# Kernel optimization log

Measured on AMD Instinct MI355X. Metric: run time of the kernel, lower is better.

Reference implementation:

```python
import jax, jax.numpy as jnp
import numpy as np

N_NODES = 10000
N_EDGES = 640000
N_GRAPHS = 64
IN_FEATS = 128
H_FEATS = 128


def setup_inputs() -> dict:
    key = jax.random.key(0)
    ks = jax.random.split(key, 8)
    in_feat = jax.random.normal(ks[0], (N_NODES, IN_FEATS), dtype=jnp.float32)
    src = jax.random.randint(ks[1], (N_EDGES,), 0, N_NODES, dtype=jnp.int32)
    dst = jax.random.randint(ks[2], (N_EDGES,), 0, N_NODES, dtype=jnp.int32)
    graph_ids = jnp.sort(jax.random.randint(ks[3], (N_NODES,), 0, N_GRAPHS, dtype=jnp.int32))
    s1 = 1.0 / np.sqrt(IN_FEATS)
    s2 = 1.0 / np.sqrt(H_FEATS)
    W1 = jax.random.uniform(ks[4], (IN_FEATS, H_FEATS), jnp.float32, -s1, s1)
    b1 = jnp.zeros((H_FEATS,), jnp.float32)
    W2 = jax.random.uniform(ks[5], (H_FEATS, H_FEATS), jnp.float32, -s2, s2)
    b2 = jnp.zeros((H_FEATS,), jnp.float32)
    Wd = jax.random.uniform(ks[6], (H_FEATS, 1), jnp.float32, -s2, s2)
    bd = jnp.zeros((1,), jnp.float32)
    return {"in_feat": in_feat, "src": src, "dst": dst, "graph_ids": graph_ids,
            "W1": W1, "b1": b1, "W2": W2, "b2": b2, "Wd": Wd, "bd": bd}


def _graph_conv(x, src, dst, norm_src, norm_dst, W, b):
    # DGL GraphConv, norm='both': D_dst^{-1/2} A D_src^{-1/2} X W + b
    x = x * norm_src[:, None]
    agg = jax.ops.segment_sum(x[src], dst, num_segments=N_NODES)  # scatter-add over edges
    agg = agg * norm_dst[:, None]
    return agg @ W + b


def reference(in_feat, src, dst, graph_ids, W1, b1, W2, b2, Wd, bd):
    ones_e = jnp.ones((N_EDGES,), in_feat.dtype)
    out_deg = jax.ops.segment_sum(ones_e, src, num_segments=N_NODES)
    in_deg = jax.ops.segment_sum(ones_e, dst, num_segments=N_NODES)
    norm_src = jnp.where(out_deg > 0, out_deg, 1.0) ** -0.5
    norm_dst = jnp.where(in_deg > 0, in_deg, 1.0) ** -0.5

    h = jax.nn.relu(_graph_conv(in_feat, src, dst, norm_src, norm_dst, W1, b1))
    h = jax.nn.relu(_graph_conv(h, src, dst, norm_src, norm_dst, W2, b2))

    # dgl.mean_nodes: per-graph mean of node features
    counts = jax.ops.segment_sum(jnp.ones((N_NODES,), h.dtype), graph_ids, num_segments=N_GRAPHS)
    pooled = jax.ops.segment_sum(h, graph_ids, num_segments=N_GRAPHS)
    pooled = pooled / jnp.maximum(counts, 1.0)[:, None]

    out = pooled @ Wd + bd  # [G, 1]
    return out.squeeze(-1)
```

## Files before the change

kernel.cpp:

```cpp
#include <hip/hip_runtime.h>
#include <hip/hip_fp16.h>

#define N_NODES 10000
#define N_EDGES 640000
#define N_GRAPHS 64
#define FEATS 128

#define NSLICE 64
#define EPS (N_EDGES / NSLICE)
#define CAP 128
#define PRE_BLOCKS 1250

static inline size_t align_up(size_t x, size_t a) { return (x + a - 1) & ~(a - 1); }

__global__ __launch_bounds__(256) void hist_kernel(const int* __restrict__ src,
                                                   const int* __restrict__ dst,
                                                   unsigned short* __restrict__ counts,
                                                   unsigned short* __restrict__ scounts,
                                                   int* __restrict__ graph_cnt,
                                                   float* __restrict__ graph_sum) {
    __shared__ int h[N_NODES];
    const int tid = threadIdx.x;
    const int b = blockIdx.x;
    if (b == 0 && tid < 2 * N_GRAPHS) {
        if (tid < N_GRAPHS) graph_cnt[tid] = 0;
        else                graph_sum[tid - N_GRAPHS] = 0.f;
    }
    const bool is_dst = (b < NSLICE);
    const int slice = is_dst ? b : b - NSLICE;
    const int* col = is_dst ? dst : src;
    unsigned short* outp = (is_dst ? counts : scounts) + slice * N_NODES;

    for (int i = tid; i < N_NODES; i += 256) h[i] = 0;
    __syncthreads();
    const int4* c4 = (const int4*)(col + slice * EPS);
    for (int i = tid; i < EPS / 4; i += 256) {
        int4 v = c4[i];
        atomicAdd(&h[v.x], 1);
        atomicAdd(&h[v.y], 1);
        atomicAdd(&h[v.z], 1);
        atomicAdd(&h[v.w], 1);
    }
    __syncthreads();
    for (int i = tid; i < N_NODES; i += 256) outp[i] = (unsigned short)h[i];
}

__global__ __launch_bounds__(256) void degnorm_base_kernel(const unsigned short* __restrict__ counts,
                                                           const unsigned short* __restrict__ scounts,
                                                           const int* __restrict__ gids,
                                                           int* __restrict__ bases,
                                                           int* __restrict__ deg_in,
                                                           float* __restrict__ norm_src,
                                                           float* __restrict__ norm_dst,
                                                           int* __restrict__ graph_cnt) {
    __shared__ int gcnt[N_GRAPHS];
    const int tid = threadIdx.x;
    if (tid < N_GRAPHS) gcnt[tid] = 0;
    __syncthreads();
    int n = blockIdx.x * 256 + tid;
    if (n < N_NODES) {
        int run = n * CAP;
        for (int s = 0; s < NSLICE; s++) {
            int c = counts[s * N_NODES + n];
            bases[s * N_NODES + n] = run;
            run += c;
        }
        int di = run - n * CAP;
        int dou = 0;
        for (int s = 0; s < NSLICE; s++) dou += scounts[s * N_NODES + n];
        deg_in[n] = di;
        norm_dst[n] = rsqrtf((float)(di < 1 ? 1 : di));
        norm_src[n] = rsqrtf((float)(dou < 1 ? 1 : dou));
        atomicAdd(&gcnt[gids[n]], 1);
    }
    __syncthreads();
    if (tid < N_GRAPHS && gcnt[tid]) atomicAdd(&graph_cnt[tid], gcnt[tid]);
}

__global__ __launch_bounds__(256) void scatter_prescale_kernel(const int* __restrict__ src,
                                                               const int* __restrict__ dst,
                                                               const int* __restrict__ bases,
                                                               int* __restrict__ sorted_src,
                                                               const float* __restrict__ in_feat,
                                                               const float* __restrict__ norm_src,
                                                               __half* __restrict__ xs) {
    const int tid = threadIdx.x;
    if (blockIdx.x < NSLICE) {
        __shared__ int cur[N_NODES];
        const int s = blockIdx.x;
        for (int i = tid; i < N_NODES; i += 256) cur[i] = bases[s * N_NODES + i];
        __syncthreads();
        const int4* s4 = (const int4*)(src + s * EPS);
        const int4* d4 = (const int4*)(dst + s * EPS);
        for (int i = tid; i < EPS / 4; i += 256) {
            int4 sv = s4[i];
            int4 dv = d4[i];
            int p;
            p = atomicAdd(&cur[dv.x], 1); sorted_src[p] = sv.x;
            p = atomicAdd(&cur[dv.y], 1); sorted_src[p] = sv.y;
            p = atomicAdd(&cur[dv.z], 1); sorted_src[p] = sv.z;
            p = atomicAdd(&cur[dv.w], 1); sorted_src[p] = sv.w;
        }
    } else {
        int i = (blockIdx.x - NSLICE) * 256 + tid;
        if (i < N_NODES * (FEATS / 4)) {
            int n = i >> 5;
            float4 v = ((const float4*)in_feat)[i];
            float s = norm_src[n];
            __half2 h0 = __floats2half2_rn(v.x * s, v.y * s);
            __half2 h1 = __floats2half2_rn(v.z * s, v.w * s);
            __half2* o = (__half2*)(xs + (size_t)i * 4);
            o[0] = h0; o[1] = h1;
        }
    }
}

__global__ __launch_bounds__(256) void aggregate_kernel(const __half* __restrict__ X,
                                                        const int* __restrict__ sorted_src,
                                                        const int* __restrict__ deg_in,
                                                        const float* __restrict__ norm_dst,
                                                        __half* __restrict__ out) {
    const int tid = threadIdx.x;
    const int wave = tid >> 6, lane = tid & 63;
    const int grp = lane >> 4, l16 = lane & 15;
    const int n = blockIdx.x * 4 + wave;
    const int start = n * CAP;
    const int cnt = deg_in[n];
    const uint4* __restrict__ x4 = (const uint4*)X;
    float acc[8] = {0.f, 0.f, 0.f, 0.f, 0.f, 0.f, 0.f, 0.f};

    int c = grp;
    for (; c + 12 < cnt; c += 16) {
        int idx[4];
#pragma unroll
        for (int k = 0; k < 4; k++) idx[k] = sorted_src[start + c + 4 * k];
        uint4 v[4];
#pragma unroll
        for (int k = 0; k < 4; k++) v[k] = x4[idx[k] * 16 + l16];
#pragma unroll
        for (int k = 0; k < 4; k++) {
            const __half2* hp = (const __half2*)&v[k];
#pragma unroll
            for (int j = 0; j < 4; j++) {
                float2 f = __half22float2(hp[j]);
                acc[2 * j]     += f.x;
                acc[2 * j + 1] += f.y;
            }
        }
    }
    for (; c < cnt; c += 4) {
        uint4 v = x4[sorted_src[start + c] * 16 + l16];
        const __half2* hp = (const __half2*)&v;
#pragma unroll
        for (int j = 0; j < 4; j++) {
            float2 f = __half22float2(hp[j]);
            acc[2 * j]     += f.x;
            acc[2 * j + 1] += f.y;
        }
    }
#pragma unroll
    for (int j = 0; j < 8; j++) {
        acc[j] += __shfl_xor(acc[j], 16);
        acc[j] += __shfl_xor(acc[j], 32);
    }
    if (grp == 0) {
        const float nd = norm_dst[n];
        __half2 o[4];
#pragma unroll
        for (int j = 0; j < 4; j++)
            o[j] = __floats2half2_rn(acc[2 * j] * nd, acc[2 * j + 1] * nd);
        *(uint4*)(out + (size_t)n * FEATS + l16 * 8) = *(const uint4*)o;
    }
}

__device__ __forceinline__ void stage_fp16_tile(const __half* __restrict__ A,
                                                int nb, int tid, float* As) {
    const int row = tid >> 4, c16 = tid & 15;
    uint4 v = *(const uint4*)(A + (size_t)(nb + row) * FEATS + c16 * 8);
    const __half2* hp = (const __half2*)&v;
    float* dst = As + row * FEATS + c16 * 8;
#pragma unroll
    for (int j = 0; j < 4; j++) {
        float2 f = __half22float2(hp[j]);
        dst[2 * j]     = f.x;
        dst[2 * j + 1] = f.y;
    }
}

__global__ __launch_bounds__(256) void gemm_relu_scale_kernel(const __half* __restrict__ A,
                                                              const float* __restrict__ W,
                                                              const float* __restrict__ bias,
                                                              const float* __restrict__ scale,
                                                              __half* __restrict__ out) {
    __shared__ float As[16 * FEATS];
    int tid = threadIdx.x;
    int nb = blockIdx.x * 16;
    stage_fp16_tile(A, nb, tid, As);
    __syncthreads();
    int fg = (tid & 31) << 2;
    int r  = tid >> 5;
    const float* a0p = As + r * FEATS;
    const float* a1p = As + (r + 8) * FEATS;
    float4 acc0 = make_float4(0.f, 0.f, 0.f, 0.f);
    float4 acc1 = make_float4(0.f, 0.f, 0.f, 0.f);
#pragma unroll 4
    for (int k = 0; k < FEATS; k++) {
        float a0 = a0p[k];
        float a1 = a1p[k];
        float4 w = *(const float4*)(W + k * FEATS + fg);
        acc0.x = fmaf(a0, w.x, acc0.x); acc0.y = fmaf(a0, w.y, acc0.y);
        acc0.z = fmaf(a0, w.z, acc0.z); acc0.w = fmaf(a0, w.w, acc0.w);
        acc1.x = fmaf(a1, w.x, acc1.x); acc1.y = fmaf(a1, w.y, acc1.y);
        acc1.z = fmaf(a1, w.z, acc1.z); acc1.w = fmaf(a1, w.w, acc1.w);
    }
    float4 bb = *(const float4*)(bias + fg);
    int gn0 = nb + r, gn1 = nb + r + 8;
    float s0 = scale[gn0], s1 = scale[gn1];
    __half2 h00 = __floats2half2_rn(fmaxf(acc0.x + bb.x, 0.f) * s0,
                                    fmaxf(acc0.y + bb.y, 0.f) * s0);
    __half2 h01 = __floats2half2_rn(fmaxf(acc0.z + bb.z, 0.f) * s0,
                                    fmaxf(acc0.w + bb.w, 0.f) * s0);
    __half2 h10 = __floats2half2_rn(fmaxf(acc1.x + bb.x, 0.f) * s1,
                                    fmaxf(acc1.y + bb.y, 0.f) * s1);
    __half2 h11 = __floats2half2_rn(fmaxf(acc1.z + bb.z, 0.f) * s1,
                                    fmaxf(acc1.w + bb.w, 0.f) * s1);
    __half2* o0 = (__half2*)(out + (size_t)gn0 * FEATS + fg);
    __half2* o1 = (__half2*)(out + (size_t)gn1 * FEATS + fg);
    o0[0] = h00; o0[1] = h01;
    o1[0] = h10; o1[1] = h11;
}

__global__ __launch_bounds__(256) void gemm_relu_pool_kernel(const __half* __restrict__ A,
                                                             const float* __restrict__ W,
                                                             const float* __restrict__ bias,
                                                             const float* __restrict__ Wd,
                                                             const int* __restrict__ gids,
                                                             float* __restrict__ graph_sum) {
    __shared__ float As[16 * FEATS];
    __shared__ float bins[N_GRAPHS];
    int tid = threadIdx.x;
    int nb = blockIdx.x * 16;
    stage_fp16_tile(A, nb, tid, As);
    if (tid < N_GRAPHS) bins[tid] = 0.f;
    __syncthreads();
    int fg = (tid & 31) << 2;
    int r  = tid >> 5;
    const float* a0p = As + r * FEATS;
    const float* a1p = As + (r + 8) * FEATS;
    float4 acc0 = make_float4(0.f, 0.f, 0.f, 0.f);
    float4 acc1 = make_float4(0.f, 0.f, 0.f, 0.f);
#pragma unroll 4
    for (int k = 0; k < FEATS; k++) {
        float a0 = a0p[k];
        float a1 = a1p[k];
        float4 w = *(const float4*)(W + k * FEATS + fg);
        acc0.x = fmaf(a0, w.x, acc0.x); acc0.y = fmaf(a0, w.y, acc0.y);
        acc0.z = fmaf(a0, w.z, acc0.z); acc0.w = fmaf(a0, w.w, acc0.w);
        acc1.x = fmaf(a1, w.x, acc1.x); acc1.y = fmaf(a1, w.y, acc1.y);
        acc1.z = fmaf(a1, w.z, acc1.z); acc1.w = fmaf(a1, w.w, acc1.w);
    }
    float4 bb = *(const float4*)(bias + fg);
    float4 wd = *(const float4*)(Wd + fg);
    float p0 = fmaxf(acc0.x + bb.x, 0.f) * wd.x + fmaxf(acc0.y + bb.y, 0.f) * wd.y +
               fmaxf(acc0.z + bb.z, 0.f) * wd.z + fmaxf(acc0.w + bb.w, 0.f) * wd.w;
    float p1 = fmaxf(acc1.x + bb.x, 0.f) * wd.x + fmaxf(acc1.y + bb.y, 0.f) * wd.y +
               fmaxf(acc1.z + bb.z, 0.f) * wd.z + fmaxf(acc1.w + bb.w, 0.f) * wd.w;
#pragma unroll
    for (int d = 16; d >= 1; d >>= 1) {
        p0 += __shfl_down(p0, d);
        p1 += __shfl_down(p1, d);
    }
    if ((tid & 31) == 0) {
        int gn0 = nb + r, gn1 = nb + r + 8;
        atomicAdd(&bins[gids[gn0]], p0);
        atomicAdd(&bins[gids[gn1]], p1);
    }
    __syncthreads();
    if (tid < N_GRAPHS) {
        float v = bins[tid];
        if (v != 0.f) atomicAdd(&graph_sum[tid], v);
    }
}

__global__ __launch_bounds__(64) void final_kernel(const float* __restrict__ graph_sum,
                                                   const int* __restrict__ graph_cnt,
                                                   const float* __restrict__ bd,
                                                   float* __restrict__ out) {
    int g = threadIdx.x;
    if (g < N_GRAPHS) {
        out[g] = graph_sum[g] / fmaxf((float)graph_cnt[g], 1.f) + bd[0];
    }
}

extern "C" void kernel_launch(void* const* d_in, const int* in_sizes, int n_in,
                              void* d_out, int out_size, void* d_ws, size_t ws_size,
                              hipStream_t stream) {
    const float* in_feat = (const float*)d_in[0];
    const int*   src     = (const int*)d_in[1];
    const int*   dst     = (const int*)d_in[2];
    const int*   gids    = (const int*)d_in[3];
    const float* W1      = (const float*)d_in[4];
    const float* b1      = (const float*)d_in[5];
    const float* W2      = (const float*)d_in[6];
    const float* b2      = (const float*)d_in[7];
    const float* Wd      = (const float*)d_in[8];
    const float* bd      = (const float*)d_in[9];
    float* out = (float*)d_out;

    char* ws = (char*)d_ws;
    size_t off = 0;
    int* graph_cnt = (int*)(ws + off); off += N_GRAPHS * 4;
    float* graph_sum = (float*)(ws + off); off += N_GRAPHS * 4;
    off = align_up(off, 512);
    unsigned short* counts  = (unsigned short*)(ws + off); off += (size_t)NSLICE * N_NODES * 2;
    off = align_up(off, 512);
    unsigned short* scounts = (unsigned short*)(ws + off); off += (size_t)NSLICE * N_NODES * 2;
    off = align_up(off, 512);
    int* bases = (int*)(ws + off); off += (size_t)NSLICE * N_NODES * 4;
    off = align_up(off, 512);
    int* deg_in  = (int*)(ws + off); off += N_NODES * 4;
    off = align_up(off, 512);
    float* norm_src = (float*)(ws + off); off += N_NODES * 4;
    off = align_up(off, 512);
    float* norm_dst = (float*)(ws + off); off += N_NODES * 4;
    off = align_up(off, 512);
    int* sorted_src = (int*)(ws + off); off += (size_t)N_NODES * CAP * 4 + 4096;
    off = align_up(off, 512);
    __half* xs   = (__half*)(ws + off); off += (size_t)N_NODES * FEATS * 2;
    off = align_up(off, 512);
    __half* h    = (__half*)(ws + off); off += (size_t)N_NODES * FEATS * 2;
    off = align_up(off, 512);
    __half* agg1 = (__half*)(ws + off); off += (size_t)N_NODES * FEATS * 2;
    off = align_up(off, 512);
    __half* agg2 = (__half*)(ws + off); off += (size_t)N_NODES * FEATS * 2;
    (void)ws_size;

    hist_kernel<<<2 * NSLICE, 256, 0, stream>>>(src, dst, counts, scounts,
                                                graph_cnt, graph_sum);
    degnorm_base_kernel<<<(N_NODES + 255) / 256, 256, 0, stream>>>(counts, scounts, gids,
                                                                   bases, deg_in, norm_src,
                                                                   norm_dst, graph_cnt);
    scatter_prescale_kernel<<<NSLICE + PRE_BLOCKS, 256, 0, stream>>>(src, dst, bases,
                                                                     sorted_src, in_feat,
                                                                     norm_src, xs);

    aggregate_kernel<<<N_NODES / 4, 256, 0, stream>>>(xs, sorted_src, deg_in, norm_dst, agg1);
    gemm_relu_scale_kernel<<<N_NODES / 16, 256, 0, stream>>>(agg1, W1, b1, norm_src, h);

    aggregate_kernel<<<N_NODES / 4, 256, 0, stream>>>(h, sorted_src, deg_in, norm_dst, agg2);
    gemm_relu_pool_kernel<<<N_NODES / 16, 256, 0, stream>>>(agg2, W2, b2, Wd, gids, graph_sum);

    final_kernel<<<1, 64, 0, stream>>>(graph_sum, graph_cnt, bd, out);
}
```

Measured before the change: 168.8 us.

## Fuse neighbor aggregation into the GEMM kernels and double histogram slices

Each layer's gather-aggregate is merged into the GEMM kernel. Every wave aggregates 4 destination nodes straight into the fp32 shared tile, so the fp16 agg1/agg2 intermediate buffers and two kernel launches go away. NSLICE is doubled to 128, which spreads the histogram and scatter work across more blocks, and degnorm is relaunched with 64-thread blocks to get more blocks. The trade-offs: the fused kernels launch only 625 blocks, each wave handles 4 nodes in sequence, so gather parallelism drops. The extra slices also make degnorm's serial per-node loop twice as long.

Result: no change. 169.3 us (+0.3%).

```diff
diff --git a/kernel.cpp b/kernel.cpp
--- a/kernel.cpp
+++ b/kernel.cpp
@@ -6,7 +6,7 @@
 #define N_GRAPHS 64
 #define FEATS 128
 
-#define NSLICE 64
+#define NSLICE 128
 #define EPS (N_EDGES / NSLICE)
 #define CAP 128
 #define PRE_BLOCKS 1250
@@ -45,19 +45,19 @@
     for (int i = tid; i < N_NODES; i += 256) outp[i] = (unsigned short)h[i];
 }
 
-__global__ __launch_bounds__(256) void degnorm_base_kernel(const unsigned short* __restrict__ counts,
-                                                           const unsigned short* __restrict__ scounts,
-                                                           const int* __restrict__ gids,
-                                                           int* __restrict__ bases,
-                                                           int* __restrict__ deg_in,
-                                                           float* __restrict__ norm_src,
-                                                           float* __restrict__ norm_dst,
-                                                           int* __restrict__ graph_cnt) {
+__global__ __launch_bounds__(64) void degnorm_base_kernel(const unsigned short* __restrict__ counts,
+                                                          const unsigned short* __restrict__ scounts,
+                                                          const int* __restrict__ gids,
+                                                          int* __restrict__ bases,
+                                                          int* __restrict__ deg_in,
+                                                          float* __restrict__ norm_src,
+                                                          float* __restrict__ norm_dst,
+                                                          int* __restrict__ graph_cnt) {
     __shared__ int gcnt[N_GRAPHS];
     const int tid = threadIdx.x;
-    if (tid < N_GRAPHS) gcnt[tid] = 0;
-    __syncthreads();
-    int n = blockIdx.x * 256 + tid;
+    gcnt[tid] = 0;
+    __syncthreads();
+    int n = blockIdx.x * 64 + tid;
     if (n < N_NODES) {
         int run = n * CAP;
         for (int s = 0; s < NSLICE; s++) {
@@ -74,7 +74,7 @@
         atomicAdd(&gcnt[gids[n]], 1);
     }
     __syncthreads();
-    if (tid < N_GRAPHS && gcnt[tid]) atomicAdd(&graph_cnt[tid], gcnt[tid]);
+    if (gcnt[tid]) atomicAdd(&graph_cnt[tid], gcnt[tid]);
 }
 
 __global__ __launch_bounds__(256) void scatter_prescale_kernel(const int* __restrict__ src,
@@ -115,15 +115,13 @@
     }
 }
 
-__global__ __launch_bounds__(256) void aggregate_kernel(const __half* __restrict__ X,
-                                                        const int* __restrict__ sorted_src,
-                                                        const int* __restrict__ deg_in,
-                                                        const float* __restrict__ norm_dst,
-                                                        __half* __restrict__ out) {
-    const int tid = threadIdx.x;
-    const int wave = tid >> 6, lane = tid & 63;
+__device__ __forceinline__ void wave_aggregate(const __half* __restrict__ X,
+                                               const int* __restrict__ sorted_src,
+                                               const int* __restrict__ deg_in,
+                                               const float* __restrict__ norm_dst,
+                                               int n, int lane,
+                                               float* __restrict__ As_row) {
     const int grp = lane >> 4, l16 = lane & 15;
-    const int n = blockIdx.x * 4 + wave;
     const int start = n * CAP;
     const int cnt = deg_in[n];
     const uint4* __restrict__ x4 = (const uint4*)X;
@@ -165,37 +163,30 @@
     }
     if (grp == 0) {
         const float nd = norm_dst[n];
-        __half2 o[4];
-#pragma unroll
-        for (int j = 0; j < 4; j++)
-            o[j] = __floats2half2_rn(acc[2 * j] * nd, acc[2 * j + 1] * nd);
-        *(uint4*)(out + (size_t)n * FEATS + l16 * 8) = *(const uint4*)o;
-    }
-}
-
-__device__ __forceinline__ void stage_fp16_tile(const __half* __restrict__ A,
-                                                int nb, int tid, float* As) {
-    const int row = tid >> 4, c16 = tid & 15;
-    uint4 v = *(const uint4*)(A + (size_t)(nb + row) * FEATS + c16 * 8);
-    const __half2* hp = (const __half2*)&v;
-    float* dst = As + row * FEATS + c16 * 8;
-#pragma unroll
-    for (int j = 0; j < 4; j++) {
-        float2 f = __half22float2(hp[j]);
-        dst[2 * j]     = f.x;
-        dst[2 * j + 1] = f.y;
-    }
-}
-
-__global__ __launch_bounds__(256) void gemm_relu_scale_kernel(const __half* __restrict__ A,
-                                                              const float* __restrict__ W,
-                                                              const float* __restrict__ bias,
-                                                              const float* __restrict__ scale,
-                                                              __half* __restrict__ out) {
+        float4 f0 = make_float4(acc[0] * nd, acc[1] * nd, acc[2] * nd, acc[3] * nd);
+        float4 f1 = make_float4(acc[4] * nd, acc[5] * nd, acc[6] * nd, acc[7] * nd);
+        *(float4*)(As_row + l16 * 8)     = f0;
+        *(float4*)(As_row + l16 * 8 + 4) = f1;
+    }
+}
+
+__global__ __launch_bounds__(256) void fused_layer1_kernel(const __half* __restrict__ xs,
+                                                           const int* __restrict__ sorted_src,
+                                                           const int* __restrict__ deg_in,
+                                                           const float* __restrict__ norm_dst,
+                                                           const float* __restrict__ W,
+                                                           const float* __restrict__ bias,
+                                                           const float* __restrict__ scale,
+                                                           __half* __restrict__ out) {
     __shared__ float As[16 * FEATS];
-    int tid = threadIdx.x;
-    int nb = blockIdx.x * 16;
-    stage_fp16_tile(A, nb, tid, As);
+    const int tid = threadIdx.x;
+    const int nb = blockIdx.x * 16;
+    const int wave = tid >> 6, lane = tid & 63;
+#pragma unroll
+    for (int i = 0; i < 4; i++) {
+        int ln = wave * 4 + i;
+        wave_aggregate(xs, sorted_src, deg_in, norm_dst, nb + ln, lane, As + ln * FEATS);
+    }
     __syncthreads();
     int fg = (tid & 31) << 2;
     int r  = tid >> 5;
@@ -230,18 +221,26 @@
     o1[0] = h10; o1[1] = h11;
 }
 
-__global__ __launch_bounds__(256) void gemm_relu_pool_kernel(const __half* __restrict__ A,
-                                                             const float* __restrict__ W,
-                                                             const float* __restrict__ bias,
-                                                             const float* __restrict__ Wd,
-                                                             const int* __restrict__ gids,
-                                                             float* __restrict__ graph_sum) {
+__global__ __launch_bounds__(256) void fused_layer2_kernel(const __half* __restrict__ h,
+                                                           const int* __restrict__ sorted_src,
+                                                           const int* __restrict__ deg_in,
+                                                           const float* __restrict__ norm_dst,
+                                                           const float* __restrict__ W,
+                                                           const float* __restrict__ bias,
+                                                           const float* __restrict__ Wd,
+                                                           const int* __restrict__ gids,
+                                                           float* __restrict__ graph_sum) {
     __shared__ float As[16 * FEATS];
     __shared__ float bins[N_GRAPHS];
-    int tid = threadIdx.x;
-    int nb = blockIdx.x * 16;
-    stage_fp16_tile(A, nb, tid, As);
+    const int tid = threadIdx.x;
+    const int nb = blockIdx.x * 16;
+    const int wave = tid >> 6, lane = tid & 63;
     if (tid < N_GRAPHS) bins[tid] = 0.f;
+#pragma unroll
+    for (int i = 0; i < 4; i++) {
+        int ln = wave * 4 + i;
+        wave_aggregate(h, sorted_src, deg_in, norm_dst, nb + ln, lane, As + ln * FEATS);
+    }
     __syncthreads();
     int fg = (tid & 31) << 2;
     int r  = tid >> 5;
@@ -329,26 +328,21 @@
     __half* xs   = (__half*)(ws + off); off += (size_t)N_NODES * FEATS * 2;
     off = align_up(off, 512);
     __half* h    = (__half*)(ws + off); off += (size_t)N_NODES * FEATS * 2;
-    off = align_up(off, 512);
-    __half* agg1 = (__half*)(ws + off); off += (size_t)N_NODES * FEATS * 2;
-    off = align_up(off, 512);
-    __half* agg2 = (__half*)(ws + off); off += (size_t)N_NODES * FEATS * 2;
     (void)ws_size;
 
     hist_kernel<<<2 * NSLICE, 256, 0, stream>>>(src, dst, counts, scounts,
                                                 graph_cnt, graph_sum);
-    degnorm_base_kernel<<<(N_NODES + 255) / 256, 256, 0, stream>>>(counts, scounts, gids,
-                                                                   bases, deg_in, norm_src,
-                                                                   norm_dst, graph_cnt);
+    degnorm_base_kernel<<<(N_NODES + 63) / 64, 64, 0, stream>>>(counts, scounts, gids,
+                                                                bases, deg_in, norm_src,
+                                                                norm_dst, graph_cnt);
     scatter_prescale_kernel<<<NSLICE + PRE_BLOCKS, 256, 0, stream>>>(src, dst, bases,
                                                                      sorted_src, in_feat,
                                                                      norm_src, xs);
 
-    aggregate_kernel<<<N_NODES / 4, 256, 0, stream>>>(xs, sorted_src, deg_in, norm_dst, agg1);
-    gemm_relu_scale_kernel<<<N_NODES / 16, 256, 0, stream>>>(agg1, W1, b1, norm_src, h);
-
-    aggregate_kernel<<<N_NODES / 4, 256, 0, stream>>>(h, sorted_src, deg_in, norm_dst, agg2);
-    gemm_relu_pool_kernel<<<N_NODES / 16, 256, 0, stream>>>(agg2, W2, b2, Wd, gids, graph_sum);
+    fused_layer1_kernel<<<N_NODES / 16, 256, 0, stream>>>(xs, sorted_src, deg_in, norm_dst,
+                                                          W1, b1, norm_src, h);
+    fused_layer2_kernel<<<N_NODES / 16, 256, 0, stream>>>(h, sorted_src, deg_in, norm_dst,
+                                                          W2, b2, Wd, gids, graph_sum);
 
     final_kernel<<<1, 64, 0, stream>>>(graph_sum, graph_cnt, bd, out);
 }
```
